# Optimization experiments

Hardware: AMD Instinct MI355X
Metric: run time of the kernel (lower is better)

The kernel has to match this reference:

```python
import jax, jax.numpy as jnp
import numpy as np

N_NODES = 100000
N_EDGES = 1600000
IN_DIM = 128
HID_DIM = 64
OUT_DIM = 1


def setup_inputs() -> dict:
    key = jax.random.key(0)
    k = jax.random.split(key, 8)
    x = jax.random.normal(k[0], (N_NODES, IN_DIM), dtype=jnp.float32)
    edge_index = jax.random.randint(k[1], (2, N_EDGES), 0, N_NODES, dtype=jnp.int64)
    # GCNConv layer 1: weight [IN, HID], bias [HID] (glorot-ish scale)
    W1 = jax.random.normal(k[2], (IN_DIM, HID_DIM), dtype=jnp.float32) / np.sqrt(IN_DIM)
    b1 = jnp.zeros((HID_DIM,), dtype=jnp.float32)
    W2 = jax.random.normal(k[3], (HID_DIM, HID_DIM), dtype=jnp.float32) / np.sqrt(HID_DIM)
    b2 = jnp.zeros((HID_DIM,), dtype=jnp.float32)
    Wfc = jax.random.normal(k[4], (HID_DIM, OUT_DIM), dtype=jnp.float32) / np.sqrt(HID_DIM)
    bfc = jnp.zeros((OUT_DIM,), dtype=jnp.float32)
    return {"x": x, "edge_index": edge_index, "W1": W1, "b1": b1,
            "W2": W2, "b2": b2, "Wfc": Wfc, "bfc": bfc}


def _gcn_norm(edge_index, n_nodes):
    # PyG GCNConv default: add self-loops, symmetric normalization.
    src, dst = edge_index[0], edge_index[1]
    loop = jnp.arange(n_nodes, dtype=src.dtype)
    src = jnp.concatenate([src, loop])
    dst = jnp.concatenate([dst, loop])
    deg = jax.ops.segment_sum(jnp.ones_like(dst, dtype=jnp.float32), dst,
                              num_segments=n_nodes)
    deg_isqrt = jax.lax.rsqrt(deg)  # deg >= 1 thanks to self-loops
    norm = deg_isqrt[src] * deg_isqrt[dst]  # [E+N]
    return src, dst, norm


def _gcn_conv(x, src, dst, norm, W, b, n_nodes):
    h = x @ W                      # [N, D_out] dense transform first (D_out <= D_in)
    msg = h[src] * norm[:, None]   # gather + normalize  [E+N, D_out]
    out = jax.ops.segment_sum(msg, dst, num_segments=n_nodes)  # scatter-add
    return out + b


def reference(x, edge_index, W1, b1, W2, b2, Wfc, bfc):
    n = x.shape[0]
    src, dst, norm = _gcn_norm(edge_index, n)
    h = jax.nn.relu(_gcn_conv(x, src, dst, norm, W1, b1, n))
    h = jax.nn.relu(_gcn_conv(h, src, dst, norm, W2, b2, n))
    return h @ Wfc + bfc  # [N, 1]
```

## Files before the change

kernel.cpp:

```cpp
#include <hip/hip_runtime.h>


#define IN_DIM 128
#define HID 64
#define B1 256
#define MAXNC 512

typedef unsigned int uint;
typedef unsigned short ushort;
typedef __attribute__((ext_vector_type(8))) short short8;
typedef __attribute__((ext_vector_type(4))) float f32x4;

__device__ inline uint pack_bf16x2(float a, float b) {
    uint ua = __builtin_bit_cast(uint, a);
    uint ub = __builtin_bit_cast(uint, b);
    ua += 0x7fffu + ((ua >> 16) & 1u);
    ub += 0x7fffu + ((ub >> 16) & 1u);
    return (ua >> 16) | (ub & 0xffff0000u);
}
__device__ inline float bf_lo(uint g) { return __builtin_bit_cast(float, g << 16); }
__device__ inline float bf_hi(uint g) { return __builtin_bit_cast(float, g & 0xffff0000u); }
__device__ inline uint rne_hi_bits(float a) {
    uint u = __builtin_bit_cast(uint, a);
    return (u + 0x7fffu + ((u >> 16) & 1u)) & 0xffff0000u;
}
__device__ inline float bitf(uint u) { return __builtin_bit_cast(float, u); }

__global__ __launch_bounds__(512) void hist1(const int* __restrict__ dst,
                                             int* __restrict__ ghist,
                                             int E, int NC, int chunk) {
    __shared__ int h[MAXNC];
    int t = threadIdx.x, blk = blockIdx.x;
    if (t < NC) h[t] = 0;
    __syncthreads();
    int s = blk * chunk, e = min(E, s + chunk);
    for (int i = s + t; i < e; i += 512) atomicAdd(&h[dst[i] >> 8], 1);
    __syncthreads();
    if (t < NC) ghist[(size_t)t * B1 + blk] = h[t];
}

__global__ __launch_bounds__(256) void scan_p1(const int* __restrict__ a,
                                               int* __restrict__ bsum, int M) {
    int i = blockIdx.x * 256 + threadIdx.x;
    int v = (i < M) ? a[i] : 0;
#pragma unroll
    for (int o = 32; o; o >>= 1) v += __shfl_down(v, o, 64);
    __shared__ int ws[4];
    int lane = threadIdx.x & 63, wid = threadIdx.x >> 6;
    if (lane == 0) ws[wid] = v;
    __syncthreads();
    if (threadIdx.x == 0) bsum[blockIdx.x] = ws[0] + ws[1] + ws[2] + ws[3];
}

__global__ __launch_bounds__(512) void scan_p2(const int* __restrict__ bsum,
                                               int* __restrict__ boff,
                                               int* __restrict__ row_off,
                                               int nb, int N,
                                               const float* __restrict__ W1f,
                                               const float* __restrict__ W2f,
                                               ushort* __restrict__ w1h,
                                               ushort* __restrict__ w1l,
                                               ushort* __restrict__ w2h,
                                               ushort* __restrict__ w2l) {
    int t = threadIdx.x;
    {
        int c = t & 63;
        int kb1 = (t >> 6) * 16;
#pragma unroll 4
        for (int kk = 0; kk < 16; ++kk) {
            int k = kb1 + kk;
            float v = W1f[k * 64 + c];
            uint rh = rne_hi_bits(v);
            w1h[c * 128 + k] = (ushort)(rh >> 16);
            w1l[c * 128 + k] = (ushort)(rne_hi_bits(v - bitf(rh)) >> 16);
        }
        int kb2 = (t >> 6) * 8;
#pragma unroll 4
        for (int kk = 0; kk < 8; ++kk) {
            int k = kb2 + kk;
            float v = W2f[k * 64 + c];
            uint rh = rne_hi_bits(v);
            w2h[c * 64 + k] = (ushort)(rh >> 16);
            w2l[c * 64 + k] = (ushort)(rne_hi_bits(v - bitf(rh)) >> 16);
        }
    }
    __shared__ int s[512];
    int v = (t < nb) ? bsum[t] : 0;
    s[t] = v;
    __syncthreads();
#pragma unroll
    for (int o = 1; o < 512; o <<= 1) {
        int add = (t >= o) ? s[t - o] : 0;
        __syncthreads();
        s[t] += add;
        __syncthreads();
    }
    if (t < nb) boff[t] = s[t] - v;
    if (t == nb - 1) row_off[N] = s[t];
}

__global__ __launch_bounds__(256) void scan_p3(int* __restrict__ a,
                                               const int* __restrict__ boff, int M) {
    __shared__ int s[256];
    int i = blockIdx.x * 256 + threadIdx.x;
    int t = threadIdx.x;
    int d = (i < M) ? a[i] : 0;
    s[t] = d;
    __syncthreads();
#pragma unroll
    for (int o = 1; o < 256; o <<= 1) {
        int add = (t >= o) ? s[t - o] : 0;
        __syncthreads();
        s[t] += add;
        __syncthreads();
    }
    if (i < M) a[i] = s[t] - d + boff[blockIdx.x];
}

__global__ __launch_bounds__(512) void scatter1(const int* __restrict__ src,
                                                const int* __restrict__ dst,
                                                const int* __restrict__ goff,
                                                uint* __restrict__ pairs,
                                                int E, int NC, int chunk) {
    __shared__ int cur[MAXNC];
    int t = threadIdx.x, blk = blockIdx.x;
    if (t < NC) cur[t] = goff[(size_t)t * B1 + blk];
    __syncthreads();
    int s = blk * chunk, e = min(E, s + chunk);
    for (int i = s + t; i < e; i += 512) {
        int d = dst[i];
        int p = atomicAdd(&cur[d >> 8], 1);
        pairs[p] = ((uint)src[i] << 8) | (uint)(d & 255);
    }
}

__global__ __launch_bounds__(256) void build_csr(const uint* __restrict__ pairs,
                                                 const int* __restrict__ goff,
                                                 int* __restrict__ row_off,
                                                 float* __restrict__ disqrt,
                                                 int* __restrict__ col,
                                                 int E, int NC, int N) {
    __shared__ int h[256], cur[256];
    __shared__ int ws[4], wsoff[4];
    int b = blockIdx.x, t = threadIdx.x;
    int base = goff[(size_t)b * B1];
    int next = (b + 1 < NC) ? goff[(size_t)(b + 1) * B1] : E;
    h[t] = 0;
    __syncthreads();
    for (int i = base + t; i < next; i += 256)
        atomicAdd(&h[pairs[i] & 255u], 1);
    __syncthreads();
    int deg = h[t];
    int incl = deg;
#pragma unroll
    for (int o = 1; o < 64; o <<= 1) {
        int u = __shfl_up(incl, o, 64);
        if ((t & 63) >= o) incl += u;
    }
    if ((t & 63) == 63) ws[t >> 6] = incl;
    __syncthreads();
    if (t == 0) {
        int run = 0;
#pragma unroll
        for (int i = 0; i < 4; ++i) { wsoff[i] = run; run += ws[i]; }
    }
    __syncthreads();
    int excl = wsoff[t >> 6] + incl - deg;
    cur[t] = base + excl;
    int node = (b << 8) + t;
    if (node < N) {
        row_off[node] = base + excl;
        disqrt[node]  = rsqrtf((float)(deg + 1));
    }
    __syncthreads();
    for (int i = base + t; i < next; i += 256) {
        uint p = pairs[i];
        int pos = atomicAdd(&cur[p & 255u], 1);
        col[pos] = (int)(p >> 8);
    }
}

template <int K, bool SPLIT>
__global__ __launch_bounds__(256) void gemm_mfma(const void* __restrict__ Xv,
                                                 const ushort* __restrict__ WHt,
                                                 const ushort* __restrict__ WLt,
                                                 const float* __restrict__ disqrt,
                                                 uint* __restrict__ Tsb, int n) {
    __shared__ ushort XH[128 * 40];
    __shared__ ushort WH[64 * 40];
    __shared__ ushort WL[64 * 40];
    __shared__ ushort XL[SPLIT ? 128 * 40 : 64];

    const int tid = threadIdx.x;
    const int m0  = blockIdx.x * 128;
    const float* Xf = (const float*)Xv;
    const char*  Xb = (const char*)Xv;

    const int wc = tid >> 2, wslot = tid & 3;
    const char* wh_g = (const char*)WHt + wc * (K * 2) + wslot * 16;
    const char* wl_g = (const char*)WLt + wc * (K * 2) + wslot * 16;

    constexpr int NL = SPLIT ? 4 : 2;
    int xr[NL], xk[NL];
#pragma unroll
    for (int i = 0; i < NL; ++i) {
        int f = tid + i * 256;
        if (SPLIT) { xr[i] = f >> 3; xk[i] = f & 7; }
        else       { xr[i] = f >> 2; xk[i] = f & 3; }
    }

    const float4 z4 = make_float4(0.f, 0.f, 0.f, 0.f);
    const uint4  zu = make_uint4(0u, 0u, 0u, 0u);
    float4 gx[NL];
    uint4  gxb[NL];
    uint4  gwh, gwl;
#pragma unroll
    for (int i = 0; i < NL; ++i) {
        int row = m0 + xr[i];
        if (SPLIT) gx[i]  = (row < n) ? *(const float4*)(Xf + (size_t)row * K + 4 * xk[i]) : z4;
        else       gxb[i] = (row < n) ? *(const uint4*)(Xb + (size_t)row * (K * 2) + xk[i] * 16) : zu;
    }
    gwh = *(const uint4*)wh_g;
    gwl = *(const uint4*)wl_g;

    f32x4 acc[2][4] = {};
    const int l   = tid & 63, wv = tid >> 6;
    const int lr  = l & 15;
    const int kob = (l >> 4) * 16;

    for (int kc = 0;;) {
        if (SPLIT) {
#pragma unroll
            for (int i = 0; i < NL; ++i) {
                float a = gx[i].x, b = gx[i].y, c = gx[i].z, d = gx[i].w;
                uint rha = rne_hi_bits(a), rhb = rne_hi_bits(b);
                uint rhc = rne_hi_bits(c), rhd = rne_hi_bits(d);
                uint2 hh, ll;
                hh.x = (rha >> 16) | (rhb & 0xffff0000u);
                hh.y = (rhc >> 16) | (rhd & 0xffff0000u);
                ll.x = pack_bf16x2(a - bitf(rha), b - bitf(rhb));
                ll.y = pack_bf16x2(c - bitf(rhc), d - bitf(rhd));
                *(uint2*)((char*)XH + xr[i] * 80 + xk[i] * 8) = hh;
                *(uint2*)((char*)XL + xr[i] * 80 + xk[i] * 8) = ll;
            }
        } else {
#pragma unroll
            for (int i = 0; i < NL; ++i)
                *(uint4*)((char*)XH + xr[i] * 80 + xk[i] * 16) = gxb[i];
        }
        *(uint4*)((char*)WH + wc * 80 + wslot * 16) = gwh;
        *(uint4*)((char*)WL + wc * 80 + wslot * 16) = gwl;
        __syncthreads();

        kc += 32;
        const bool more = kc < K;
        if (more) {
#pragma unroll
            for (int i = 0; i < NL; ++i) {
                int row = m0 + xr[i];
                if (SPLIT) gx[i]  = (row < n) ? *(const float4*)(Xf + (size_t)row * K + kc + 4 * xk[i]) : z4;
                else       gxb[i] = (row < n) ? *(const uint4*)(Xb + (size_t)row * (K * 2) + kc * 2 + xk[i] * 16) : zu;
            }
            gwh = *(const uint4*)(wh_g + kc * 2);
            gwl = *(const uint4*)(wl_g + kc * 2);
        }

        short8 xh0 = *(const short8*)((const char*)XH + (wv * 32 + 0 + lr) * 80 + kob);
        short8 xh1 = *(const short8*)((const char*)XH + (wv * 32 + 16 + lr) * 80 + kob);
        short8 xl0, xl1;
        if (SPLIT) {
            xl0 = *(const short8*)((const char*)XL + (wv * 32 + 0 + lr) * 80 + kob);
            xl1 = *(const short8*)((const char*)XL + (wv * 32 + 16 + lr) * 80 + kob);
        }
#pragma unroll
        for (int nn = 0; nn < 4; ++nn) {
            short8 wh = *(const short8*)((const char*)WH + (nn * 16 + lr) * 80 + kob);
            short8 wl = *(const short8*)((const char*)WL + (nn * 16 + lr) * 80 + kob);
            acc[0][nn] = __builtin_amdgcn_mfma_f32_16x16x32_bf16(wh, xh0, acc[0][nn], 0, 0, 0);
            acc[1][nn] = __builtin_amdgcn_mfma_f32_16x16x32_bf16(wh, xh1, acc[1][nn], 0, 0, 0);
            acc[0][nn] = __builtin_amdgcn_mfma_f32_16x16x32_bf16(wl, xh0, acc[0][nn], 0, 0, 0);
            acc[1][nn] = __builtin_amdgcn_mfma_f32_16x16x32_bf16(wl, xh1, acc[1][nn], 0, 0, 0);
            if (SPLIT) {
                acc[0][nn] = __builtin_amdgcn_mfma_f32_16x16x32_bf16(wh, xl0, acc[0][nn], 0, 0, 0);
                acc[1][nn] = __builtin_amdgcn_mfma_f32_16x16x32_bf16(wh, xl1, acc[1][nn], 0, 0, 0);
            }
        }
        if (!more) break;
        __syncthreads();
    }

#pragma unroll
    for (int m = 0; m < 2; ++m) {
        int node = m0 + wv * 32 + m * 16 + lr;
        if (node < n) {
            float dq = disqrt[node];
#pragma unroll
            for (int nn = 0; nn < 4; ++nn) {
                f32x4 a = acc[m][nn];
                uint2 pk;
                pk.x = pack_bf16x2(a[0] * dq, a[1] * dq);
                pk.y = pack_bf16x2(a[2] * dq, a[3] * dq);
                *(uint2*)((char*)Tsb + (size_t)node * 128 + nn * 32 + (l >> 4) * 8) = pk;
            }
        }
    }
}

template <bool FUSE_FC>
__global__ __launch_bounds__(256) void agg_kernel(const uint* __restrict__ Tsb,
                                                  const int* __restrict__ row_off,
                                                  const int* __restrict__ col,
                                                  const float* __restrict__ disqrt,
                                                  const float* __restrict__ bias,
                                                  const float* __restrict__ wfc,
                                                  const float* __restrict__ bfc,
                                                  uint* __restrict__ outb,
                                                  float* __restrict__ outf,
                                                  int node0, int nhi) {
    int node = node0 + blockIdx.x * 4 + (threadIdx.x >> 6);
    if (node >= nhi) return;
    int lane = threadIdx.x & 63;
    int o = lane >> 3;
    int p = lane & 7;
    float acc[8] = {};
    if (o == 0) {
        uint4 g = *(const uint4*)(Tsb + (size_t)node * 32 + 4 * p);
        acc[0] = bf_lo(g.x); acc[1] = bf_hi(g.x);
        acc[2] = bf_lo(g.y); acc[3] = bf_hi(g.y);
        acc[4] = bf_lo(g.z); acc[5] = bf_hi(g.z);
        acc[6] = bf_lo(g.w); acc[7] = bf_hi(g.w);
    }
    int beg = __builtin_amdgcn_readfirstlane(row_off[node]);
    int end = __builtin_amdgcn_readfirstlane(row_off[node + 1]);
    for (int batch = beg; batch < end; batch += 64) {
        int bn = min(64, end - batch);
        int cv = 0;
        if (batch + lane < end) cv = col[batch + lane];
        int j = 0;
        for (; j + 16 <= bn; j += 16) {
            int s0 = __shfl(cv, j + o, 64);
            int s1 = __shfl(cv, j + 8 + o, 64);
            uint4 g0 = *(const uint4*)(Tsb + (size_t)s0 * 32 + 4 * p);
            uint4 g1 = *(const uint4*)(Tsb + (size_t)s1 * 32 + 4 * p);
            acc[0] += bf_lo(g0.x); acc[1] += bf_hi(g0.x);
            acc[2] += bf_lo(g0.y); acc[3] += bf_hi(g0.y);
            acc[4] += bf_lo(g0.z); acc[5] += bf_hi(g0.z);
            acc[6] += bf_lo(g0.w); acc[7] += bf_hi(g0.w);
            acc[0] += bf_lo(g1.x); acc[1] += bf_hi(g1.x);
            acc[2] += bf_lo(g1.y); acc[3] += bf_hi(g1.y);
            acc[4] += bf_lo(g1.z); acc[5] += bf_hi(g1.z);
            acc[6] += bf_lo(g1.w); acc[7] += bf_hi(g1.w);
        }
        for (; j < bn; j += 8) {
            int idx = j + o;
            int s = __shfl(cv, idx & 63, 64);
            uint4 g = *(const uint4*)(Tsb + (size_t)s * 32 + 4 * p);
            if (idx < bn) {
                acc[0] += bf_lo(g.x); acc[1] += bf_hi(g.x);
                acc[2] += bf_lo(g.y); acc[3] += bf_hi(g.y);
                acc[4] += bf_lo(g.z); acc[5] += bf_hi(g.z);
                acc[6] += bf_lo(g.w); acc[7] += bf_hi(g.w);
            }
        }
    }
#pragma unroll
    for (int k = 0; k < 8; ++k) {
        acc[k] += __shfl_xor(acc[k], 8, 64);
        acc[k] += __shfl_xor(acc[k], 16, 64);
        acc[k] += __shfl_xor(acc[k], 32, 64);
    }
    float dq = disqrt[node];
    float4 bv0 = *(const float4*)(bias + 8 * p);
    float4 bv1 = *(const float4*)(bias + 8 * p + 4);
    float r[8];
    r[0] = fmaxf(acc[0] * dq + bv0.x, 0.f);
    r[1] = fmaxf(acc[1] * dq + bv0.y, 0.f);
    r[2] = fmaxf(acc[2] * dq + bv0.z, 0.f);
    r[3] = fmaxf(acc[3] * dq + bv0.w, 0.f);
    r[4] = fmaxf(acc[4] * dq + bv1.x, 0.f);
    r[5] = fmaxf(acc[5] * dq + bv1.y, 0.f);
    r[6] = fmaxf(acc[6] * dq + bv1.z, 0.f);
    r[7] = fmaxf(acc[7] * dq + bv1.w, 0.f);
    if (!FUSE_FC) {
        if (o == 0) {
            uint4 pk;
            pk.x = pack_bf16x2(r[0], r[1]);
            pk.y = pack_bf16x2(r[2], r[3]);
            pk.z = pack_bf16x2(r[4], r[5]);
            pk.w = pack_bf16x2(r[6], r[7]);
            *(uint4*)(outb + (size_t)node * 32 + 4 * p) = pk;
        }
    } else {
        float4 wv0 = *(const float4*)(wfc + 8 * p);
        float4 wv1 = *(const float4*)(wfc + 8 * p + 4);
        float v = r[0] * wv0.x + r[1] * wv0.y + r[2] * wv0.z + r[3] * wv0.w +
                  r[4] * wv1.x + r[5] * wv1.y + r[6] * wv1.z + r[7] * wv1.w;
        v += __shfl_down(v, 4, 64);
        v += __shfl_down(v, 2, 64);
        v += __shfl_down(v, 1, 64);
        if (lane == 0) outf[node] = v + bfc[0];
    }
}

extern "C" void kernel_launch(void* const* d_in, const int* in_sizes, int n_in,
                              void* d_out, int out_size, void* d_ws, size_t ws_size,
                              hipStream_t stream) {
    const float* x   = (const float*)d_in[0];
    const int*   ei  = (const int*)d_in[1];
    const float* W1  = (const float*)d_in[2];
    const float* b1  = (const float*)d_in[3];
    const float* W2  = (const float*)d_in[4];
    const float* b2  = (const float*)d_in[5];
    const float* Wfc = (const float*)d_in[6];
    const float* bfc = (const float*)d_in[7];
    float* out = (float*)d_out;

    const int N = in_sizes[0] / IN_DIM;
    const int E = in_sizes[1] / 2;
    const int* src = ei;
    const int* dst = ei + E;
    const int NC    = (N + 255) >> 8;
    const int chunk = (E + B1 - 1) / B1;
    const int M     = NC * B1;
    const int NBs   = (M + 255) / 256;

    char* w = (char*)d_ws;
    auto alloc = [&](size_t bytes) {
        void* p = (void*)w;
        w += (bytes + 255) & ~(size_t)255;
        return p;
    };
    int*   row_off = (int*)alloc((size_t)(N + 1) * 4);
    float* disqrt  = (float*)alloc((size_t)N * 4);
    int*   goff    = (int*)alloc((size_t)NC * B1 * 4);
    int*   bsum    = (int*)alloc(512 * 4);
    int*   boff    = (int*)alloc(512 * 4);
    int*   col     = (int*)alloc((size_t)E * 4);
    ushort* w1h    = (ushort*)alloc(64 * 128 * 2);
    ushort* w1l    = (ushort*)alloc(64 * 128 * 2);
    ushort* w2h    = (ushort*)alloc(64 * 64 * 2);
    ushort* w2l    = (ushort*)alloc(64 * 64 * 2);
    size_t scrA = (size_t)E * 4, scrB = (size_t)N * HID * 2;
    void*  scr  = alloc(scrA > scrB ? scrA : scrB);
    uint*  h1b  = (uint*)alloc((size_t)N * HID * 2);
    uint*  pairs = (uint*)scr;
    uint*  Tsb   = (uint*)scr;

    hist1<<<B1, 512, 0, stream>>>(dst, goff, E, NC, chunk);
    scan_p1<<<NBs, 256, 0, stream>>>(goff, bsum, M);
    scan_p2<<<1, 512, 0, stream>>>(bsum, boff, row_off, NBs, N,
                                   W1, W2, w1h, w1l, w2h, w2l);
    scan_p3<<<NBs, 256, 0, stream>>>(goff, boff, M);
    scatter1<<<B1, 512, 0, stream>>>(src, dst, goff, pairs, E, NC, chunk);
    build_csr<<<NC, 256, 0, stream>>>(pairs, goff, row_off, disqrt, col, E, NC, N);

    gemm_mfma<IN_DIM, true><<<(N + 127) / 128, 256, 0, stream>>>(
        x, w1h, w1l, disqrt, Tsb, N);
    agg_kernel<false><<<(N + 3) / 4, 256, 0, stream>>>(Tsb, row_off, col, disqrt,
                                                       b1, nullptr, nullptr,
                                                       h1b, nullptr, 0, N);

    gemm_mfma<HID, false><<<(N + 127) / 128, 256, 0, stream>>>(
        h1b, w2h, w2l, disqrt, Tsb, N);
    agg_kernel<true><<<(N + 3) / 4, 256, 0, stream>>>(Tsb, row_off, col, disqrt,
                                                      b2, Wfc, bfc,
                                                      nullptr, out, 0, N);
}
```

Measured before the change: 265.5 us.

## Fuse CSR build pipeline into one cooperative kernel with grid syncs

New measurement: 499.1 us. 1.88x slower.

```diff
diff --git a/kernel.cpp b/kernel.cpp
--- a/kernel.cpp
+++ b/kernel.cpp
@@ -1,4 +1,7 @@
 #include <hip/hip_runtime.h>
+#include <hip/hip_cooperative_groups.h>
+
+namespace cg = cooperative_groups;
 
 
 #define IN_DIM 128
@@ -26,157 +29,149 @@
 }
 __device__ inline float bitf(uint u) { return __builtin_bit_cast(float, u); }
 
-__global__ __launch_bounds__(512) void hist1(const int* __restrict__ dst,
-                                             int* __restrict__ ghist,
-                                             int E, int NC, int chunk) {
-    __shared__ int h[MAXNC];
-    int t = threadIdx.x, blk = blockIdx.x;
-    if (t < NC) h[t] = 0;
-    __syncthreads();
-    int s = blk * chunk, e = min(E, s + chunk);
-    for (int i = s + t; i < e; i += 512) atomicAdd(&h[dst[i] >> 8], 1);
-    __syncthreads();
-    if (t < NC) ghist[(size_t)t * B1 + blk] = h[t];
-}
-
-__global__ __launch_bounds__(256) void scan_p1(const int* __restrict__ a,
-                                               int* __restrict__ bsum, int M) {
-    int i = blockIdx.x * 256 + threadIdx.x;
-    int v = (i < M) ? a[i] : 0;
-#pragma unroll
-    for (int o = 32; o; o >>= 1) v += __shfl_down(v, o, 64);
-    __shared__ int ws[4];
-    int lane = threadIdx.x & 63, wid = threadIdx.x >> 6;
-    if (lane == 0) ws[wid] = v;
-    __syncthreads();
-    if (threadIdx.x == 0) bsum[blockIdx.x] = ws[0] + ws[1] + ws[2] + ws[3];
-}
-
-__global__ __launch_bounds__(512) void scan_p2(const int* __restrict__ bsum,
-                                               int* __restrict__ boff,
-                                               int* __restrict__ row_off,
-                                               int nb, int N,
-                                               const float* __restrict__ W1f,
-                                               const float* __restrict__ W2f,
-                                               ushort* __restrict__ w1h,
-                                               ushort* __restrict__ w1l,
-                                               ushort* __restrict__ w2h,
-                                               ushort* __restrict__ w2l) {
-    int t = threadIdx.x;
-    {
-        int c = t & 63;
-        int kb1 = (t >> 6) * 16;
-#pragma unroll 4
-        for (int kk = 0; kk < 16; ++kk) {
-            int k = kb1 + kk;
-            float v = W1f[k * 64 + c];
+__global__ __launch_bounds__(512, 4) void coop_build(
+        const int* __restrict__ src, const int* __restrict__ dst,
+        int* __restrict__ ghist,
+        int* __restrict__ bsum, int* __restrict__ boff,
+        uint* __restrict__ pairs,
+        int* __restrict__ row_off, float* __restrict__ disqrt,
+        int* __restrict__ col,
+        int E, int NC, int N, int chunk,
+        const float* __restrict__ W1f, const float* __restrict__ W2f,
+        ushort* __restrict__ w1h, ushort* __restrict__ w1l,
+        ushort* __restrict__ w2h, ushort* __restrict__ w2l) {
+    cg::grid_group grid = cg::this_grid();
+    __shared__ int sh[520];
+    const int t = threadIdx.x;
+    const int b = blockIdx.x;
+    const int M = NC * B1;
+    const int NBs = (M + 255) >> 8;
+
+    if (b < B1) {
+        for (int i = t; i < NC; i += 512) sh[i] = 0;
+        __syncthreads();
+        int s = b * chunk, e = min(E, s + chunk);
+        for (int i = s + t; i < e; i += 512) atomicAdd(&sh[dst[i] >> 8], 1);
+        __syncthreads();
+        for (int i = t; i < NC; i += 512) ghist[(size_t)i * B1 + b] = sh[i];
+    } else if (b == B1) {
+        for (int i = t; i < 128 * 64; i += 512) {
+            int k = i >> 6, c = i & 63;
+            float v = W1f[i];
             uint rh = rne_hi_bits(v);
             w1h[c * 128 + k] = (ushort)(rh >> 16);
             w1l[c * 128 + k] = (ushort)(rne_hi_bits(v - bitf(rh)) >> 16);
         }
-        int kb2 = (t >> 6) * 8;
-#pragma unroll 4
-        for (int kk = 0; kk < 8; ++kk) {
-            int k = kb2 + kk;
-            float v = W2f[k * 64 + c];
+    } else if (b == B1 + 1) {
+        for (int i = t; i < 64 * 64; i += 512) {
+            int k = i >> 6, c = i & 63;
+            float v = W2f[i];
             uint rh = rne_hi_bits(v);
             w2h[c * 64 + k] = (ushort)(rh >> 16);
             w2l[c * 64 + k] = (ushort)(rne_hi_bits(v - bitf(rh)) >> 16);
         }
     }
-    __shared__ int s[512];
-    int v = (t < nb) ? bsum[t] : 0;
-    s[t] = v;
-    __syncthreads();
-#pragma unroll
-    for (int o = 1; o < 512; o <<= 1) {
-        int add = (t >= o) ? s[t - o] : 0;
-        __syncthreads();
-        s[t] += add;
-        __syncthreads();
-    }
-    if (t < nb) boff[t] = s[t] - v;
-    if (t == nb - 1) row_off[N] = s[t];
-}
-
-__global__ __launch_bounds__(256) void scan_p3(int* __restrict__ a,
-                                               const int* __restrict__ boff, int M) {
-    __shared__ int s[256];
-    int i = blockIdx.x * 256 + threadIdx.x;
-    int t = threadIdx.x;
-    int d = (i < M) ? a[i] : 0;
-    s[t] = d;
-    __syncthreads();
-#pragma unroll
-    for (int o = 1; o < 256; o <<= 1) {
-        int add = (t >= o) ? s[t - o] : 0;
-        __syncthreads();
-        s[t] += add;
-        __syncthreads();
-    }
-    if (i < M) a[i] = s[t] - d + boff[blockIdx.x];
-}
-
-__global__ __launch_bounds__(512) void scatter1(const int* __restrict__ src,
-                                                const int* __restrict__ dst,
-                                                const int* __restrict__ goff,
-                                                uint* __restrict__ pairs,
-                                                int E, int NC, int chunk) {
-    __shared__ int cur[MAXNC];
-    int t = threadIdx.x, blk = blockIdx.x;
-    if (t < NC) cur[t] = goff[(size_t)t * B1 + blk];
-    __syncthreads();
-    int s = blk * chunk, e = min(E, s + chunk);
-    for (int i = s + t; i < e; i += 512) {
-        int d = dst[i];
-        int p = atomicAdd(&cur[d >> 8], 1);
-        pairs[p] = ((uint)src[i] << 8) | (uint)(d & 255);
-    }
-}
-
-__global__ __launch_bounds__(256) void build_csr(const uint* __restrict__ pairs,
-                                                 const int* __restrict__ goff,
-                                                 int* __restrict__ row_off,
-                                                 float* __restrict__ disqrt,
-                                                 int* __restrict__ col,
-                                                 int E, int NC, int N) {
-    __shared__ int h[256], cur[256];
-    __shared__ int ws[4], wsoff[4];
-    int b = blockIdx.x, t = threadIdx.x;
-    int base = goff[(size_t)b * B1];
-    int next = (b + 1 < NC) ? goff[(size_t)(b + 1) * B1] : E;
-    h[t] = 0;
-    __syncthreads();
-    for (int i = base + t; i < next; i += 256)
-        atomicAdd(&h[pairs[i] & 255u], 1);
-    __syncthreads();
-    int deg = h[t];
-    int incl = deg;
-#pragma unroll
-    for (int o = 1; o < 64; o <<= 1) {
-        int u = __shfl_up(incl, o, 64);
-        if ((t & 63) >= o) incl += u;
-    }
-    if ((t & 63) == 63) ws[t >> 6] = incl;
-    __syncthreads();
-    if (t == 0) {
-        int run = 0;
-#pragma unroll
-        for (int i = 0; i < 4; ++i) { wsoff[i] = run; run += ws[i]; }
-    }
-    __syncthreads();
-    int excl = wsoff[t >> 6] + incl - deg;
-    cur[t] = base + excl;
-    int node = (b << 8) + t;
-    if (node < N) {
-        row_off[node] = base + excl;
-        disqrt[node]  = rsqrtf((float)(deg + 1));
-    }
-    __syncthreads();
-    for (int i = base + t; i < next; i += 256) {
-        uint p = pairs[i];
-        int pos = atomicAdd(&cur[p & 255u], 1);
-        col[pos] = (int)(p >> 8);
+    grid.sync();
+
+    if (b < NBs) {
+        int idx = b * 256 + t;
+        int v = (t < 256 && idx < M) ? ghist[idx] : 0;
+#pragma unroll
+        for (int o = 32; o; o >>= 1) v += __shfl_down(v, o, 64);
+        int lane = t & 63, wid = t >> 6;
+        if (lane == 0) sh[512 - 8 + wid] = v;
+        __syncthreads();
+        if (t == 0) {
+            int s = 0;
+#pragma unroll
+            for (int i = 0; i < 8; ++i) s += sh[512 - 8 + i];
+            bsum[b] = s;
+        }
+    }
+    grid.sync();
+
+    if (b == 0) {
+        int v = (t < NBs) ? bsum[t] : 0;
+        sh[t] = v;
+        __syncthreads();
+#pragma unroll
+        for (int o = 1; o < 512; o <<= 1) {
+            int add = (t >= o) ? sh[t - o] : 0;
+            __syncthreads();
+            sh[t] += add;
+            __syncthreads();
+        }
+        if (t < NBs) boff[t] = sh[t] - v;
+        if (t == NBs - 1) row_off[N] = sh[t];
+    }
+    grid.sync();
+
+    if (b < NBs) {
+        int i = b * 256 + t;
+        int d = (t < 256 && i < M) ? ghist[i] : 0;
+        if (t < 256) sh[t] = d;
+        __syncthreads();
+#pragma unroll
+        for (int o = 1; o < 256; o <<= 1) {
+            int add = (t >= o && t < 256) ? sh[t - o] : 0;
+            __syncthreads();
+            if (t < 256) sh[t] += add;
+            __syncthreads();
+        }
+        if (t < 256 && i < M) ghist[i] = sh[t] - d + boff[b];
+    }
+    grid.sync();
+
+    if (b < B1) {
+        for (int i = t; i < NC; i += 512) sh[i] = ghist[(size_t)i * B1 + b];
+        __syncthreads();
+        int s = b * chunk, e = min(E, s + chunk);
+        for (int i = s + t; i < e; i += 512) {
+            int d = dst[i];
+            int p = atomicAdd(&sh[d >> 8], 1);
+            pairs[p] = ((uint)src[i] << 8) | (uint)(d & 255);
+        }
+    }
+    grid.sync();
+
+    if (b < NC) {
+        int base = ghist[(size_t)b * B1];
+        int next = (b + 1 < NC) ? ghist[(size_t)(b + 1) * B1] : E;
+        if (t < 256) sh[t] = 0;
+        __syncthreads();
+        for (int i = base + t; i < next; i += 512)
+            atomicAdd(&sh[pairs[i] & 255u], 1);
+        __syncthreads();
+        int deg = (t < 256) ? sh[t] : 0;
+        int incl = deg;
+#pragma unroll
+        for (int o = 1; o < 64; o <<= 1) {
+            int u = __shfl_up(incl, o, 64);
+            if ((t & 63) >= o) incl += u;
+        }
+        if (t < 256 && (t & 63) == 63) sh[512 + (t >> 6)] = incl;
+        __syncthreads();
+        if (t == 0) {
+            int run = 0;
+#pragma unroll
+            for (int i = 0; i < 4; ++i) { sh[516 + i] = run; run += sh[512 + i]; }
+        }
+        __syncthreads();
+        if (t < 256) {
+            int excl = sh[516 + (t >> 6)] + incl - deg;
+            sh[256 + t] = base + excl;
+            int node = (b << 8) + t;
+            if (node < N) {
+                row_off[node] = base + excl;
+                disqrt[node]  = rsqrtf((float)(deg + 1));
+            }
+        }
+        __syncthreads();
+        for (int i = base + t; i < next; i += 512) {
+            uint p = pairs[i];
+            int pos = atomicAdd(&sh[256 + (p & 255u)], 1);
+            col[pos] = (int)(p >> 8);
+        }
     }
 }
 
@@ -421,8 +416,6 @@
     const int* dst = ei + E;
     const int NC    = (N + 255) >> 8;
     const int chunk = (E + B1 - 1) / B1;
-    const int M     = NC * B1;
-    const int NBs   = (M + 255) / 256;
 
     char* w = (char*)d_ws;
     auto alloc = [&](size_t bytes) {
@@ -446,13 +439,17 @@
     uint*  pairs = (uint*)scr;
     uint*  Tsb   = (uint*)scr;
 
-    hist1<<<B1, 512, 0, stream>>>(dst, goff, E, NC, chunk);
-    scan_p1<<<NBs, 256, 0, stream>>>(goff, bsum, M);
-    scan_p2<<<1, 512, 0, stream>>>(bsum, boff, row_off, NBs, N,
-                                   W1, W2, w1h, w1l, w2h, w2l);
-    scan_p3<<<NBs, 256, 0, stream>>>(goff, boff, M);
-    scatter1<<<B1, 512, 0, stream>>>(src, dst, goff, pairs, E, NC, chunk);
-    build_csr<<<NC, 256, 0, stream>>>(pairs, goff, row_off, disqrt, col, E, NC, N);
+    {
+        int gridn = (NC > B1 + 2) ? NC : (B1 + 2);
+        void* kargs[] = {
+            (void*)&src, (void*)&dst, (void*)&goff, (void*)&bsum, (void*)&boff,
+            (void*)&pairs, (void*)&row_off, (void*)&disqrt, (void*)&col,
+            (void*)&E, (void*)&NC, (void*)&N, (void*)&chunk,
+            (void*)&W1, (void*)&W2,
+            (void*)&w1h, (void*)&w1l, (void*)&w2h, (void*)&w2l };
+        hipLaunchCooperativeKernel((const void*)coop_build, dim3(gridn), dim3(512),
+                                   kargs, 0, stream);
+    }
 
     gemm_mfma<IN_DIM, true><<<(N + 127) / 128, 256, 0, stream>>>(
         x, w1h, w1l, disqrt, Tsb, N);
```

## Stage scatter bucketing in LDS for coalesced writes; merge scan passes

Applied to the files above, without the earlier changes.

Result: slower. 276.3 us (+4.1%).

```diff
diff --git a/kernel.cpp b/kernel.cpp
--- a/kernel.cpp
+++ b/kernel.cpp
@@ -5,6 +5,7 @@
 #define HID 64
 #define B1 256
 #define MAXNC 512
+#define CHCAP 6400
 
 typedef unsigned int uint;
 typedef unsigned short ushort;
@@ -39,29 +40,16 @@
     if (t < NC) ghist[(size_t)t * B1 + blk] = h[t];
 }
 
-__global__ __launch_bounds__(256) void scan_p1(const int* __restrict__ a,
-                                               int* __restrict__ bsum, int M) {
-    int i = blockIdx.x * 256 + threadIdx.x;
-    int v = (i < M) ? a[i] : 0;
-#pragma unroll
-    for (int o = 32; o; o >>= 1) v += __shfl_down(v, o, 64);
-    __shared__ int ws[4];
-    int lane = threadIdx.x & 63, wid = threadIdx.x >> 6;
-    if (lane == 0) ws[wid] = v;
-    __syncthreads();
-    if (threadIdx.x == 0) bsum[blockIdx.x] = ws[0] + ws[1] + ws[2] + ws[3];
-}
-
-__global__ __launch_bounds__(512) void scan_p2(const int* __restrict__ bsum,
-                                               int* __restrict__ boff,
-                                               int* __restrict__ row_off,
-                                               int nb, int N,
-                                               const float* __restrict__ W1f,
-                                               const float* __restrict__ W2f,
-                                               ushort* __restrict__ w1h,
-                                               ushort* __restrict__ w1l,
-                                               ushort* __restrict__ w2h,
-                                               ushort* __restrict__ w2l) {
+__global__ __launch_bounds__(512) void scan_p12(const int* __restrict__ a,
+                                                int* __restrict__ boff,
+                                                int* __restrict__ row_off,
+                                                int M, int N,
+                                                const float* __restrict__ W1f,
+                                                const float* __restrict__ W2f,
+                                                ushort* __restrict__ w1h,
+                                                ushort* __restrict__ w1l,
+                                                ushort* __restrict__ w2h,
+                                                ushort* __restrict__ w2l) {
     int t = threadIdx.x;
     {
         int c = t & 63;
@@ -84,8 +72,21 @@
             w2l[c * 64 + k] = (ushort)(rne_hi_bits(v - bitf(rh)) >> 16);
         }
     }
+    const int nb = (M + 255) >> 8;
+    int v = 0;
+    if (t < nb) {
+        int base = t * 256, end = min(M, base + 256);
+        const int4* p4 = (const int4*)(a + base);
+        int4 sa = make_int4(0, 0, 0, 0);
+        int q4 = (end - base) >> 2;
+        for (int k = 0; k < q4; ++k) {
+            int4 q = p4[k];
+            sa.x += q.x; sa.y += q.y; sa.z += q.z; sa.w += q.w;
+        }
+        v = sa.x + sa.y + sa.z + sa.w;
+        for (int r = base + (q4 << 2); r < end; ++r) v += a[r];
+    }
     __shared__ int s[512];
-    int v = (t < nb) ? bsum[t] : 0;
     s[t] = v;
     __syncthreads();
 #pragma unroll
@@ -122,15 +123,51 @@
                                                 const int* __restrict__ goff,
                                                 uint* __restrict__ pairs,
                                                 int E, int NC, int chunk) {
-    __shared__ int cur[MAXNC];
+    __shared__ uint   pl[CHCAP];
+    __shared__ ushort bl[CHCAP];
+    __shared__ int    lb[MAXNC];
+    __shared__ int    cu[MAXNC];
+    __shared__ int    ss[512];
     int t = threadIdx.x, blk = blockIdx.x;
-    if (t < NC) cur[t] = goff[(size_t)t * B1 + blk];
-    __syncthreads();
-    int s = blk * chunk, e = min(E, s + chunk);
-    for (int i = s + t; i < e; i += 512) {
-        int d = dst[i];
-        int p = atomicAdd(&cur[d >> 8], 1);
-        pairs[p] = ((uint)src[i] << 8) | (uint)(d & 255);
+    int s = blk * chunk, e = min(E, s + chunk), n = e - s;
+    if (chunk <= CHCAP) {
+        for (int i = t; i < NC; i += 512) lb[i] = 0;
+        __syncthreads();
+        for (int i = s + t; i < e; i += 512) atomicAdd(&lb[dst[i] >> 8], 1);
+        __syncthreads();
+        int v = (t < NC) ? lb[t] : 0;
+        ss[t] = v;
+        __syncthreads();
+#pragma unroll
+        for (int o = 1; o < 512; o <<= 1) {
+            int add = (t >= o) ? ss[t - o] : 0;
+            __syncthreads();
+            ss[t] += add;
+            __syncthreads();
+        }
+        if (t < NC) { lb[t] = ss[t] - v; cu[t] = ss[t] - v; }
+        __syncthreads();
+        for (int i = s + t; i < e; i += 512) {
+            int d = dst[i], b = d >> 8;
+            int p = atomicAdd(&cu[b], 1);
+            pl[p] = ((uint)src[i] << 8) | (uint)(d & 255);
+            bl[p] = (ushort)b;
+        }
+        __syncthreads();
+        for (int i = t; i < NC; i += 512) cu[i] = goff[(size_t)i * B1 + blk];
+        __syncthreads();
+        for (int j = t; j < n; j += 512) {
+            int b = bl[j];
+            pairs[cu[b] + (j - lb[b])] = pl[j];
+        }
+    } else {
+        for (int i = t; i < NC; i += 512) cu[i] = goff[(size_t)i * B1 + blk];
+        __syncthreads();
+        for (int i = s + t; i < e; i += 512) {
+            int d = dst[i];
+            int p = atomicAdd(&cu[d >> 8], 1);
+            pairs[p] = ((uint)src[i] << 8) | (uint)(d & 255);
+        }
     }
 }
 
@@ -433,7 +470,6 @@
     int*   row_off = (int*)alloc((size_t)(N + 1) * 4);
     float* disqrt  = (float*)alloc((size_t)N * 4);
     int*   goff    = (int*)alloc((size_t)NC * B1 * 4);
-    int*   bsum    = (int*)alloc(512 * 4);
     int*   boff    = (int*)alloc(512 * 4);
     int*   col     = (int*)alloc((size_t)E * 4);
     ushort* w1h    = (ushort*)alloc(64 * 128 * 2);
@@ -447,9 +483,8 @@
     uint*  Tsb   = (uint*)scr;
 
     hist1<<<B1, 512, 0, stream>>>(dst, goff, E, NC, chunk);
-    scan_p1<<<NBs, 256, 0, stream>>>(goff, bsum, M);
-    scan_p2<<<1, 512, 0, stream>>>(bsum, boff, row_off, NBs, N,
-                                   W1, W2, w1h, w1l, w2h, w2l);
+    scan_p12<<<1, 512, 0, stream>>>(goff, boff, row_off, M, N,
+                                    W1, W2, w1h, w1l, w2h, w2l);
     scan_p3<<<NBs, 256, 0, stream>>>(goff, boff, M);
     scatter1<<<B1, 512, 0, stream>>>(src, dst, goff, pairs, E, NC, chunk);
     build_csr<<<NC, 256, 0, stream>>>(pairs, goff, row_off, disqrt, col, E, NC, N);
```

## Replace histogram+scan CSR build with fixed-capacity bucket slack buffers

Applied to the files above, without the earlier changes.

New measurement: 256.3 us (median of 2 runs). -3.5%, faster.

```diff
diff --git a/kernel.cpp b/kernel.cpp
--- a/kernel.cpp
+++ b/kernel.cpp
@@ -5,6 +5,7 @@
 #define HID 64
 #define B1 256
 #define MAXNC 512
+#define BCAP 8192
 
 typedef unsigned int uint;
 typedef unsigned short ushort;
@@ -26,129 +27,69 @@
 }
 __device__ inline float bitf(uint u) { return __builtin_bit_cast(float, u); }
 
-__global__ __launch_bounds__(512) void hist1(const int* __restrict__ dst,
-                                             int* __restrict__ ghist,
-                                             int E, int NC, int chunk) {
-    __shared__ int h[MAXNC];
+__global__ __launch_bounds__(512) void scatter_bkt(
+        const int* __restrict__ src, const int* __restrict__ dst,
+        int* __restrict__ bktcnt, uint* __restrict__ slack,
+        int E, int NC, int chunk,
+        const float* __restrict__ W1f, const float* __restrict__ W2f,
+        ushort* __restrict__ w1h, ushort* __restrict__ w1l,
+        ushort* __restrict__ w2h, ushort* __restrict__ w2l) {
     int t = threadIdx.x, blk = blockIdx.x;
-    if (t < NC) h[t] = 0;
-    __syncthreads();
-    int s = blk * chunk, e = min(E, s + chunk);
-    for (int i = s + t; i < e; i += 512) atomicAdd(&h[dst[i] >> 8], 1);
-    __syncthreads();
-    if (t < NC) ghist[(size_t)t * B1 + blk] = h[t];
-}
-
-__global__ __launch_bounds__(256) void scan_p1(const int* __restrict__ a,
-                                               int* __restrict__ bsum, int M) {
-    int i = blockIdx.x * 256 + threadIdx.x;
-    int v = (i < M) ? a[i] : 0;
-#pragma unroll
-    for (int o = 32; o; o >>= 1) v += __shfl_down(v, o, 64);
-    __shared__ int ws[4];
-    int lane = threadIdx.x & 63, wid = threadIdx.x >> 6;
-    if (lane == 0) ws[wid] = v;
-    __syncthreads();
-    if (threadIdx.x == 0) bsum[blockIdx.x] = ws[0] + ws[1] + ws[2] + ws[3];
-}
-
-__global__ __launch_bounds__(512) void scan_p2(const int* __restrict__ bsum,
-                                               int* __restrict__ boff,
-                                               int* __restrict__ row_off,
-                                               int nb, int N,
-                                               const float* __restrict__ W1f,
-                                               const float* __restrict__ W2f,
-                                               ushort* __restrict__ w1h,
-                                               ushort* __restrict__ w1l,
-                                               ushort* __restrict__ w2h,
-                                               ushort* __restrict__ w2l) {
-    int t = threadIdx.x;
-    {
-        int c = t & 63;
-        int kb1 = (t >> 6) * 16;
-#pragma unroll 4
-        for (int kk = 0; kk < 16; ++kk) {
-            int k = kb1 + kk;
-            float v = W1f[k * 64 + c];
+    if (blk < B1) {
+        __shared__ int h[MAXNC], cur[MAXNC];
+        for (int i = t; i < NC; i += 512) h[i] = 0;
+        __syncthreads();
+        int s = blk * chunk, e = min(E, s + chunk);
+        for (int i = s + t; i < e; i += 512) atomicAdd(&h[dst[i] >> 8], 1);
+        __syncthreads();
+        for (int i = t; i < NC; i += 512)
+            cur[i] = h[i] ? atomicAdd(&bktcnt[i], h[i]) : 0;
+        __syncthreads();
+        for (int i = s + t; i < e; i += 512) {
+            int d = dst[i], b = d >> 8;
+            int p = atomicAdd(&cur[b], 1);
+            slack[(size_t)b * BCAP + p] = ((uint)src[i] << 8) | (uint)(d & 255);
+        }
+    } else if (blk == B1) {
+        for (int i = t; i < 128 * 64; i += 512) {
+            int k = i >> 6, c = i & 63;
+            float v = W1f[i];
             uint rh = rne_hi_bits(v);
             w1h[c * 128 + k] = (ushort)(rh >> 16);
             w1l[c * 128 + k] = (ushort)(rne_hi_bits(v - bitf(rh)) >> 16);
         }
-        int kb2 = (t >> 6) * 8;
-#pragma unroll 4
-        for (int kk = 0; kk < 8; ++kk) {
-            int k = kb2 + kk;
-            float v = W2f[k * 64 + c];
+    } else {
+        for (int i = t; i < 64 * 64; i += 512) {
+            int k = i >> 6, c = i & 63;
+            float v = W2f[i];
             uint rh = rne_hi_bits(v);
             w2h[c * 64 + k] = (ushort)(rh >> 16);
             w2l[c * 64 + k] = (ushort)(rne_hi_bits(v - bitf(rh)) >> 16);
         }
     }
-    __shared__ int s[512];
-    int v = (t < nb) ? bsum[t] : 0;
-    s[t] = v;
-    __syncthreads();
-#pragma unroll
-    for (int o = 1; o < 512; o <<= 1) {
-        int add = (t >= o) ? s[t - o] : 0;
-        __syncthreads();
-        s[t] += add;
-        __syncthreads();
-    }
-    if (t < nb) boff[t] = s[t] - v;
-    if (t == nb - 1) row_off[N] = s[t];
-}
-
-__global__ __launch_bounds__(256) void scan_p3(int* __restrict__ a,
-                                               const int* __restrict__ boff, int M) {
-    __shared__ int s[256];
-    int i = blockIdx.x * 256 + threadIdx.x;
-    int t = threadIdx.x;
-    int d = (i < M) ? a[i] : 0;
-    s[t] = d;
-    __syncthreads();
-#pragma unroll
-    for (int o = 1; o < 256; o <<= 1) {
-        int add = (t >= o) ? s[t - o] : 0;
-        __syncthreads();
-        s[t] += add;
-        __syncthreads();
-    }
-    if (i < M) a[i] = s[t] - d + boff[blockIdx.x];
-}
-
-__global__ __launch_bounds__(512) void scatter1(const int* __restrict__ src,
-                                                const int* __restrict__ dst,
-                                                const int* __restrict__ goff,
-                                                uint* __restrict__ pairs,
-                                                int E, int NC, int chunk) {
-    __shared__ int cur[MAXNC];
-    int t = threadIdx.x, blk = blockIdx.x;
-    if (t < NC) cur[t] = goff[(size_t)t * B1 + blk];
-    __syncthreads();
-    int s = blk * chunk, e = min(E, s + chunk);
-    for (int i = s + t; i < e; i += 512) {
-        int d = dst[i];
-        int p = atomicAdd(&cur[d >> 8], 1);
-        pairs[p] = ((uint)src[i] << 8) | (uint)(d & 255);
-    }
-}
-
-__global__ __launch_bounds__(256) void build_csr(const uint* __restrict__ pairs,
-                                                 const int* __restrict__ goff,
-                                                 int* __restrict__ row_off,
-                                                 float* __restrict__ disqrt,
-                                                 int* __restrict__ col,
-                                                 int E, int NC, int N) {
+}
+
+__global__ __launch_bounds__(256) void build_csr2(const int* __restrict__ bktcnt,
+                                                  const uint* __restrict__ slack,
+                                                  int* __restrict__ row_off,
+                                                  float* __restrict__ disqrt,
+                                                  int* __restrict__ col,
+                                                  int NC, int N) {
+    __shared__ int red[4], ws[4], wsoff[4];
     __shared__ int h[256], cur[256];
-    __shared__ int ws[4], wsoff[4];
     int b = blockIdx.x, t = threadIdx.x;
-    int base = goff[(size_t)b * B1];
-    int next = (b + 1 < NC) ? goff[(size_t)(b + 1) * B1] : E;
+    int part = 0;
+    for (int i = t; i < b; i += 256) part += bktcnt[i];
+#pragma unroll
+    for (int o = 32; o; o >>= 1) part += __shfl_down(part, o, 64);
+    if ((t & 63) == 0) red[t >> 6] = part;
     h[t] = 0;
     __syncthreads();
-    for (int i = base + t; i < next; i += 256)
-        atomicAdd(&h[pairs[i] & 255u], 1);
+    const int base = red[0] + red[1] + red[2] + red[3];
+    const int cnt  = bktcnt[b];
+    const uint* bp = slack + (size_t)b * BCAP;
+    for (int i = t; i < cnt; i += 256)
+        atomicAdd(&h[bp[i] & 255u], 1);
     __syncthreads();
     int deg = h[t];
     int incl = deg;
@@ -172,9 +113,10 @@
         row_off[node] = base + excl;
         disqrt[node]  = rsqrtf((float)(deg + 1));
     }
+    if (b == NC - 1 && t == 0) row_off[N] = base + cnt;
     __syncthreads();
-    for (int i = base + t; i < next; i += 256) {
-        uint p = pairs[i];
+    for (int i = t; i < cnt; i += 256) {
+        uint p = bp[i];
         int pos = atomicAdd(&cur[p & 255u], 1);
         col[pos] = (int)(p >> 8);
     }
@@ -421,8 +363,6 @@
     const int* dst = ei + E;
     const int NC    = (N + 255) >> 8;
     const int chunk = (E + B1 - 1) / B1;
-    const int M     = NC * B1;
-    const int NBs   = (M + 255) / 256;
 
     char* w = (char*)d_ws;
     auto alloc = [&](size_t bytes) {
@@ -432,27 +372,22 @@
     };
     int*   row_off = (int*)alloc((size_t)(N + 1) * 4);
     float* disqrt  = (float*)alloc((size_t)N * 4);
-    int*   goff    = (int*)alloc((size_t)NC * B1 * 4);
-    int*   bsum    = (int*)alloc(512 * 4);
-    int*   boff    = (int*)alloc(512 * 4);
+    int*   bktcnt  = (int*)alloc(MAXNC * 4);
     int*   col     = (int*)alloc((size_t)E * 4);
     ushort* w1h    = (ushort*)alloc(64 * 128 * 2);
     ushort* w1l    = (ushort*)alloc(64 * 128 * 2);
     ushort* w2h    = (ushort*)alloc(64 * 64 * 2);
     ushort* w2l    = (ushort*)alloc(64 * 64 * 2);
-    size_t scrA = (size_t)E * 4, scrB = (size_t)N * HID * 2;
+    size_t scrA = (size_t)NC * BCAP * 4, scrB = (size_t)N * HID * 2;
     void*  scr  = alloc(scrA > scrB ? scrA : scrB);
     uint*  h1b  = (uint*)alloc((size_t)N * HID * 2);
-    uint*  pairs = (uint*)scr;
+    uint*  slack = (uint*)scr;
     uint*  Tsb   = (uint*)scr;
 
-    hist1<<<B1, 512, 0, stream>>>(dst, goff, E, NC, chunk);
-    scan_p1<<<NBs, 256, 0, stream>>>(goff, bsum, M);
-    scan_p2<<<1, 512, 0, stream>>>(bsum, boff, row_off, NBs, N,
-                                   W1, W2, w1h, w1l, w2h, w2l);
-    scan_p3<<<NBs, 256, 0, stream>>>(goff, boff, M);
-    scatter1<<<B1, 512, 0, stream>>>(src, dst, goff, pairs, E, NC, chunk);
-    build_csr<<<NC, 256, 0, stream>>>(pairs, goff, row_off, disqrt, col, E, NC, N);
+    hipMemsetAsync(bktcnt, 0, MAXNC * 4, stream);
+    scatter_bkt<<<B1 + 2, 512, 0, stream>>>(src, dst, bktcnt, slack, E, NC, chunk,
+                                            W1, W2, w1h, w1l, w2h, w2l);
+    build_csr2<<<NC, 256, 0, stream>>>(bktcnt, slack, row_off, disqrt, col, NC, N);
 
     gemm_mfma<IN_DIM, true><<<(N + 127) / 128, 256, 0, stream>>>(
         x, w1h, w1l, disqrt, Tsb, N);
```
